# Optimization experiments

Hardware: AMD Instinct MI355X
Metric: run time of the kernel (lower is better)

## Reference

```python
import jax, jax.numpy as jnp
import numpy as np

N = 500_000
H = 256          # hidden_channels
A = 64           # aggr_channels
K = 5            # number of aggregators: sum, min, max, mean, std
B = 8192         # num graphs (segments)


def setup_inputs() -> dict:
    key = jax.random.key(0)
    k1, k2, k3, k4 = jax.random.split(key, 4)
    x = jax.random.normal(k1, (N, H), dtype=jnp.float32)
    batch = jnp.sort(jax.random.randint(k2, (N,), 0, B)).astype(jnp.int64)
    # Linear weights (stored input-major so forward is x @ W)
    W1 = jax.random.normal(k3, (H, A * K), dtype=jnp.float32) * (1.0 / np.sqrt(H))
    W2 = jax.random.normal(k4, (A * K, H), dtype=jnp.float32) * (1.0 / np.sqrt(A * K))
    b = jnp.zeros((H,), dtype=jnp.float32)
    return {"x": x, "batch": batch, "num_graphs": B, "W1": W1, "W2": W2, "b": b}


def reference(x, batch, num_graphs, W1, W2, b):
    # lin_aggr (no bias), then chunk into 5 pieces of width A along features
    h = x @ W1                                   # [N, 5A]
    h_sum, h_min, h_max, h_mean, h_std = jnp.split(h, K, axis=1)

    seg = batch.astype(jnp.int32)
    cnt = jax.ops.segment_sum(jnp.ones((x.shape[0], 1), x.dtype), seg,
                              num_segments=num_graphs)            # [B, 1]
    cnt = jnp.maximum(cnt, 1.0)

    z_sum = jax.ops.segment_sum(h_sum, seg, num_segments=num_graphs)
    z_min = jax.ops.segment_min(h_min, seg, num_segments=num_graphs)
    z_max = jax.ops.segment_max(h_max, seg, num_segments=num_graphs)
    z_mean = jax.ops.segment_sum(h_mean, seg, num_segments=num_graphs) / cnt
    # std via E[x^2] - E[x]^2 (PyG StdAggregation), clamped for stability
    m = jax.ops.segment_sum(h_std, seg, num_segments=num_graphs) / cnt
    m2 = jax.ops.segment_sum(h_std * h_std, seg, num_segments=num_graphs) / cnt
    z_std = jnp.sqrt(jnp.maximum(m2 - m * m, 1e-5))

    z = jnp.concatenate([z_sum, z_min, z_max, z_mean, z_std], axis=1)  # [B, 5A]
    return z @ W2 + b                                                   # [B, H]
```

## Files before the change

### kernel.cpp

```cpp
#include <hip/hip_runtime.h>
#include <hip/hip_bf16.h>
#include <float.h>
#include <stdint.h>

typedef __attribute__((ext_vector_type(8))) short bf16x8;
typedef __attribute__((ext_vector_type(4))) float f32x4;

#define NCH 320
#define NCG 20
#define GEMM_GRID 1024

static __device__ __forceinline__ unsigned short f2bf(float f) {
    union { float f; unsigned int u; } v; v.f = f;
    unsigned int u = v.u;
    u += 0x7FFFu + ((u >> 16) & 1u);
    return (unsigned short)(u >> 16);
}

static __device__ __forceinline__ float bf2f(unsigned short h) {
    union { unsigned int u; float f; } v; v.u = ((unsigned int)h) << 16;
    return v.f;
}

__global__ void seg_start_kernel(const int* __restrict__ batch,
                                 int* __restrict__ seg, int n, int b_gr) {
    int b = blockIdx.x * blockDim.x + threadIdx.x;
    if (b > b_gr) return;
    int lo = 0, hi = n;
    while (lo < hi) {
        int mid = (lo + hi) >> 1;
        if (batch[mid] < b) lo = mid + 1; else hi = mid;
    }
    seg[b] = lo;
}

__global__ void pack_w1_kernel(const float* __restrict__ W1,
                               unsigned short* __restrict__ w1p) {
    int idx = blockIdx.x * blockDim.x + threadIdx.x;
    if (idx >= NCG * 8 * 64) return;
    int lane = idx & 63;
    int ks = (idx >> 6) & 7;
    int cg = idx >> 9;
    int col = cg * 16 + (lane & 15);
    int kbase = ks * 32 + (lane >> 4) * 8;
    unsigned short* dst = w1p + (size_t)idx * 8;
#pragma unroll
    for (int j = 0; j < 8; ++j)
        dst[j] = f2bf(W1[(size_t)(kbase + j) * NCH + col]);
}

__global__ __launch_bounds__(512)
__attribute__((amdgpu_waves_per_eu(2, 2)))
void gemm_h_kernel(const float* __restrict__ x,
                   const unsigned short* __restrict__ w1p,
                   unsigned short* __restrict__ h,
                   int n, int nchunks, int span) {
    __shared__ unsigned short xs[64 * 256];

    const int tid = threadIdx.x;
    const int lane = tid & 63;
    const int w = tid >> 6;
    const int rg = lane >> 4;
    const int col = lane & 15;
    const int chA = w * 16 + col;
    const int chB = (w + 8) * 16 + col;
    const int chS = (16 + (w & 3)) * 16 + col;
    const int sthalf = w >> 2;

    const bf16x8* wp = (const bf16x8*)w1p;
    bf16x8 B0[8], B1[8], Bs[8];
#pragma unroll
    for (int ks = 0; ks < 8; ++ks) {
        B0[ks] = wp[(w * 8 + ks) * 64 + lane];
        B1[ks] = wp[((w + 8) * 8 + ks) * 64 + lane];
        Bs[ks] = wp[((16 + (w & 3)) * 8 + ks) * 64 + lane];
        asm volatile("" : "+v"(B0[ks]));
        asm volatile("" : "+v"(B1[ks]));
        asm volatile("" : "+v"(Bs[ks]));
    }

    int addrk[8];
#pragma unroll
    for (int ks = 0; ks < 8; ++ks)
        addrk[ks] = ((col * 512) + (rg * 16) + ks * 64) ^ ((col & 7) << 4);

    const float4* xv = (const float4*)x;
    const int c0 = blockIdx.x * span;
    const int c1 = min(c0 + span, nchunks);
    if (c0 >= c1) return;

#define LD8(CH) { const int base_ = (CH) << 6; \
        const int rem_ = min(n - base_, 64); \
        _Pragma("unroll") \
        for (int i_ = 0; i_ < 8; ++i_) { \
            int q_ = tid + i_ * 512; int row_ = q_ >> 6; \
            p[i_] = make_float4(0.f, 0.f, 0.f, 0.f); \
            if (row_ < rem_) p[i_] = xv[(size_t)(base_ + row_) * 64 + (q_ & 63)]; } }

#define ST8() { \
        _Pragma("unroll") \
        for (int i_ = 0; i_ < 8; ++i_) { \
            int q_ = tid + i_ * 512; int row_ = q_ >> 6; \
            int byt_ = ((row_ * 512) + ((q_ & 63) * 8)) ^ ((row_ & 7) << 4); \
            __hip_bfloat162 lo2_ = __float22bfloat162_rn(make_float2(p[i_].x, p[i_].y)); \
            __hip_bfloat162 hi2_ = __float22bfloat162_rn(make_float2(p[i_].z, p[i_].w)); \
            unsigned int ulo_, uhi_; \
            __builtin_memcpy(&ulo_, &lo2_, 4); __builtin_memcpy(&uhi_, &hi2_, 4); \
            *(uint2*)((char*)xs + byt_) = make_uint2(ulo_, uhi_); } }

    {
        float4 p[8];
        LD8(c0)
        ST8()
    }
    __syncthreads();

    for (int tc = c0; tc < c1; ++tc) {
        const bool more = (tc + 1 < c1);
        float4 p[8];
        if (more) LD8(tc + 1)
        const int base = tc << 6;
#pragma unroll
        for (int ps = 0; ps < 2; ++ps) {
            f32x4 aA0 = {0,0,0,0}, aA1 = {0,0,0,0};
            f32x4 aB0 = {0,0,0,0}, aB1 = {0,0,0,0};
            f32x4 aS0 = {0,0,0,0}, aS1 = {0,0,0,0};
            const char* pb = (const char*)xs + ps * 16384;
            const bool dostd = (sthalf == ps);
#pragma unroll
            for (int ks = 0; ks < 8; ++ks) {
                bf16x8 x0 = *(const bf16x8*)(pb + addrk[ks]);
                bf16x8 x1 = *(const bf16x8*)(pb + addrk[ks] + 8192);
                aA0 = __builtin_amdgcn_mfma_f32_16x16x32_bf16(x0, B0[ks], aA0, 0, 0, 0);
                aB0 = __builtin_amdgcn_mfma_f32_16x16x32_bf16(x0, B1[ks], aB0, 0, 0, 0);
                aA1 = __builtin_amdgcn_mfma_f32_16x16x32_bf16(x1, B0[ks], aA1, 0, 0, 0);
                aB1 = __builtin_amdgcn_mfma_f32_16x16x32_bf16(x1, B1[ks], aB1, 0, 0, 0);
                if (dostd) {
                    aS0 = __builtin_amdgcn_mfma_f32_16x16x32_bf16(x0, Bs[ks], aS0, 0, 0, 0);
                    aS1 = __builtin_amdgcn_mfma_f32_16x16x32_bf16(x1, Bs[ks], aS1, 0, 0, 0);
                }
            }
            const int rb0 = base + ps * 32 + rg * 4;
            const int rb1 = rb0 + 16;
            unsigned short* hp0 = h + (size_t)(rb0 >> 2) * 1280;
            unsigned short* hp1 = h + (size_t)(rb1 >> 2) * 1280;
#define STG(ACC, CH, HP) { \
            __hip_bfloat162 lo2 = __float22bfloat162_rn(make_float2((ACC)[0], (ACC)[1])); \
            __hip_bfloat162 hi2 = __float22bfloat162_rn(make_float2((ACC)[2], (ACC)[3])); \
            uint2 pk2; \
            __builtin_memcpy(&pk2.x, &lo2, 4); __builtin_memcpy(&pk2.y, &hi2, 4); \
            *(uint2*)((HP) + (CH) * 4) = pk2; }
            STG(aA0, chA, hp0)
            STG(aA1, chA, hp1)
            STG(aB0, chB, hp0)
            STG(aB1, chB, hp1)
            if (dostd) {
                STG(aS0, chS, hp0)
                STG(aS1, chS, hp1)
            }
#undef STG
        }
        __syncthreads();
        if (more) {
            ST8()
            __syncthreads();
        }
    }
#undef LD8
#undef ST8
}

__global__ __launch_bounds__(320) void reduce_kernel(
    const unsigned short* __restrict__ h, const int* __restrict__ seg,
    float* __restrict__ z) {
    const int g = blockIdx.x;
    const int sg = seg[g], en = seg[g + 1];
    const int cnt = en - sg;
    const int t = threadIdx.x;

    float s = 0.f, q = 0.f, mn = FLT_MAX, mx = -FLT_MAX;
    if (cnt > 0) {
        const unsigned short* hp = h + (size_t)t * 4;
        const int b40 = sg >> 2, b41 = (en - 1) >> 2;
        for (int b4 = b40; b4 <= b41; ++b4) {
            uint2 u = *(const uint2*)(hp + (size_t)b4 * 1280);
            const int r0 = b4 << 2;
#pragma unroll
            for (int j = 0; j < 4; ++j) {
                unsigned short e = (j < 2)
                    ? (unsigned short)((j == 0) ? (u.x & 0xFFFFu) : (u.x >> 16))
                    : (unsigned short)((j == 2) ? (u.y & 0xFFFFu) : (u.y >> 16));
                float v = bf2f(e);
                bool inr = (r0 + j >= sg) && (r0 + j < en);
                s += inr ? v : 0.f;
                q += inr ? v * v : 0.f;
                mn = fminf(mn, inr ? v : FLT_MAX);
                mx = fmaxf(mx, inr ? v : -FLT_MAX);
            }
        }
    }
    const float cntf = (float)max(cnt, 1);
    const int a = t >> 6;
    float res;
    if (a == 0) res = s;
    else if (a == 1) res = mn;
    else if (a == 2) res = mx;
    else if (a == 3) res = s / cntf;
    else {
        float m1 = s / cntf, m2 = q / cntf;
        res = sqrtf(fmaxf(m2 - m1 * m1, 1e-5f));
    }
    z[(size_t)g * NCH + t] = res;
}

__global__ __launch_bounds__(256) void k2_kernel(
    const float* __restrict__ z, const float* __restrict__ W2,
    const float* __restrict__ bias, float* __restrict__ out) {
    __shared__ float zf[NCH][17];
    const int g0 = blockIdx.x * 16;
    const int tid = threadIdx.x;
    for (int idx = tid; idx < 16 * NCH; idx += 256) {
        int m = idx / NCH;
        int c = idx - m * NCH;
        zf[c][m] = z[(size_t)(g0 + m) * NCH + c];
    }
    __syncthreads();
    float acc[16];
#pragma unroll
    for (int m = 0; m < 16; ++m) acc[m] = 0.f;
    for (int k = 0; k < NCH; ++k) {
        float wv = W2[(size_t)k * 256 + tid];
#pragma unroll
        for (int m = 0; m < 16; ++m) acc[m] += zf[k][m] * wv;
    }
    float bv = bias[tid];
#pragma unroll
    for (int m = 0; m < 16; ++m)
        out[(size_t)(g0 + m) * 256 + tid] = acc[m] + bv;
}

extern "C" void kernel_launch(void* const* d_in, const int* in_sizes, int n_in,
                              void* d_out, int out_size, void* d_ws, size_t ws_size,
                              hipStream_t stream) {
    const float* x = (const float*)d_in[0];
    const int* batch = (const int*)d_in[1];
    const float* W1 = (const float*)d_in[3];
    const float* W2 = (const float*)d_in[4];
    const float* bias = (const float*)d_in[5];

    const int n = in_sizes[1];
    const int b_gr = out_size / 256;
    const int nchunks = (n + 63) >> 6;
    const int span = (nchunks + GEMM_GRID - 1) / GEMM_GRID;

    char* ws = (char*)d_ws;
    unsigned short* w1p = (unsigned short*)ws;
    int* seg = (int*)(ws + 163840);
    float* z = (float*)(ws + 262144);
    unsigned short* h = (unsigned short*)(ws + 262144 +
                         (size_t)b_gr * NCH * sizeof(float));

    seg_start_kernel<<<(b_gr + 256) / 256, 256, 0, stream>>>(batch, seg, n, b_gr);
    pack_w1_kernel<<<(NCG * 8 * 64 + 255) / 256, 256, 0, stream>>>(W1, w1p);
    gemm_h_kernel<<<GEMM_GRID, 512, 0, stream>>>(x, w1p, h, n, nchunks, span);
    reduce_kernel<<<b_gr, 320, 0, stream>>>(h, seg, z);
    k2_kernel<<<b_gr / 16, 256, 0, stream>>>(z, W2, bias, (float*)d_out);
}
```

Before: 398.6 us.

## Double-buffer LDS tiles and prefetch two chunks ahead in GEMM kernel

Converts the GEMM's single LDS tile into two ping-pong buffers and keeps two register prefetch sets, so global loads for chunk tc+2 are in flight while chunk tc is computed. Barriers become raw s_barrier calls with lgkmcnt waits instead of __syncthreads. The grid is halved so each block runs more chunks and the deeper pipeline has more to overlap. In exchange it doubles LDS use and raises register pressure, which may limit occupancy.

```diff
diff --git a/kernel.cpp b/kernel.cpp
--- a/kernel.cpp
+++ b/kernel.cpp
@@ -8,7 +8,7 @@
 
 #define NCH 320
 #define NCG 20
-#define GEMM_GRID 1024
+#define GEMM_GRID 512
 
 static __device__ __forceinline__ unsigned short f2bf(float f) {
     union { float f; unsigned int u; } v; v.f = f;
@@ -55,7 +55,7 @@
                    const unsigned short* __restrict__ w1p,
                    unsigned short* __restrict__ h,
                    int n, int nchunks, int span) {
-    __shared__ unsigned short xs[64 * 256];
+    __shared__ unsigned short xs[2][64 * 256];
 
     const int tid = threadIdx.x;
     const int lane = tid & 63;
@@ -89,85 +89,99 @@
     const int c1 = min(c0 + span, nchunks);
     if (c0 >= c1) return;
 
-#define LD8(CH) { const int base_ = (CH) << 6; \
-        const int rem_ = min(n - base_, 64); \
+#define LGKBAR { asm volatile("s_waitcnt lgkmcnt(0)" ::: "memory"); \
+                 __builtin_amdgcn_s_barrier(); \
+                 asm volatile("" ::: "memory"); }
+
+#define LDM(P, CH) { const int ch_ = (CH); const int base_ = ch_ << 6; \
+        const int rem_ = (ch_ < c1) ? min(n - base_, 64) : 0; \
         _Pragma("unroll") \
         for (int i_ = 0; i_ < 8; ++i_) { \
             int q_ = tid + i_ * 512; int row_ = q_ >> 6; \
-            p[i_] = make_float4(0.f, 0.f, 0.f, 0.f); \
-            if (row_ < rem_) p[i_] = xv[(size_t)(base_ + row_) * 64 + (q_ & 63)]; } }
-
-#define ST8() { \
+            P[i_] = make_float4(0.f, 0.f, 0.f, 0.f); \
+            if (row_ < rem_) P[i_] = xv[(size_t)(base_ + row_) * 64 + (q_ & 63)]; } }
+
+#define STM(P, BUF) { \
         _Pragma("unroll") \
         for (int i_ = 0; i_ < 8; ++i_) { \
             int q_ = tid + i_ * 512; int row_ = q_ >> 6; \
             int byt_ = ((row_ * 512) + ((q_ & 63) * 8)) ^ ((row_ & 7) << 4); \
-            __hip_bfloat162 lo2_ = __float22bfloat162_rn(make_float2(p[i_].x, p[i_].y)); \
-            __hip_bfloat162 hi2_ = __float22bfloat162_rn(make_float2(p[i_].z, p[i_].w)); \
+            __hip_bfloat162 lo2_ = __float22bfloat162_rn(make_float2(P[i_].x, P[i_].y)); \
+            __hip_bfloat162 hi2_ = __float22bfloat162_rn(make_float2(P[i_].z, P[i_].w)); \
             unsigned int ulo_, uhi_; \
             __builtin_memcpy(&ulo_, &lo2_, 4); __builtin_memcpy(&uhi_, &hi2_, 4); \
-            *(uint2*)((char*)xs + byt_) = make_uint2(ulo_, uhi_); } }
-
-    {
-        float4 p[8];
-        LD8(c0)
-        ST8()
-    }
-    __syncthreads();
-
-    for (int tc = c0; tc < c1; ++tc) {
-        const bool more = (tc + 1 < c1);
-        float4 p[8];
-        if (more) LD8(tc + 1)
-        const int base = tc << 6;
-#pragma unroll
-        for (int ps = 0; ps < 2; ++ps) {
-            f32x4 aA0 = {0,0,0,0}, aA1 = {0,0,0,0};
-            f32x4 aB0 = {0,0,0,0}, aB1 = {0,0,0,0};
-            f32x4 aS0 = {0,0,0,0}, aS1 = {0,0,0,0};
-            const char* pb = (const char*)xs + ps * 16384;
-            const bool dostd = (sthalf == ps);
-#pragma unroll
-            for (int ks = 0; ks < 8; ++ks) {
-                bf16x8 x0 = *(const bf16x8*)(pb + addrk[ks]);
-                bf16x8 x1 = *(const bf16x8*)(pb + addrk[ks] + 8192);
-                aA0 = __builtin_amdgcn_mfma_f32_16x16x32_bf16(x0, B0[ks], aA0, 0, 0, 0);
-                aB0 = __builtin_amdgcn_mfma_f32_16x16x32_bf16(x0, B1[ks], aB0, 0, 0, 0);
-                aA1 = __builtin_amdgcn_mfma_f32_16x16x32_bf16(x1, B0[ks], aA1, 0, 0, 0);
-                aB1 = __builtin_amdgcn_mfma_f32_16x16x32_bf16(x1, B1[ks], aB1, 0, 0, 0);
-                if (dostd) {
-                    aS0 = __builtin_amdgcn_mfma_f32_16x16x32_bf16(x0, Bs[ks], aS0, 0, 0, 0);
-                    aS1 = __builtin_amdgcn_mfma_f32_16x16x32_bf16(x1, Bs[ks], aS1, 0, 0, 0);
-                }
-            }
-            const int rb0 = base + ps * 32 + rg * 4;
-            const int rb1 = rb0 + 16;
-            unsigned short* hp0 = h + (size_t)(rb0 >> 2) * 1280;
-            unsigned short* hp1 = h + (size_t)(rb1 >> 2) * 1280;
+            *(uint2*)((char*)(xs[BUF]) + byt_) = make_uint2(ulo_, uhi_); } }
+
+#define COMPUTE(TC, BUF) { \
+        const int base = (TC) << 6; \
+        _Pragma("unroll") \
+        for (int ps = 0; ps < 2; ++ps) { \
+            f32x4 aA0 = {0,0,0,0}, aA1 = {0,0,0,0}; \
+            f32x4 aB0 = {0,0,0,0}, aB1 = {0,0,0,0}; \
+            f32x4 aS0 = {0,0,0,0}, aS1 = {0,0,0,0}; \
+            const char* pb = (const char*)(xs[BUF]) + ps * 16384; \
+            const bool dostd = (sthalf == ps); \
+            _Pragma("unroll") \
+            for (int ks = 0; ks < 8; ++ks) { \
+                bf16x8 x0 = *(const bf16x8*)(pb + addrk[ks]); \
+                bf16x8 x1 = *(const bf16x8*)(pb + addrk[ks] + 8192); \
+                aA0 = __builtin_amdgcn_mfma_f32_16x16x32_bf16(x0, B0[ks], aA0, 0, 0, 0); \
+                aB0 = __builtin_amdgcn_mfma_f32_16x16x32_bf16(x0, B1[ks], aB0, 0, 0, 0); \
+                aA1 = __builtin_amdgcn_mfma_f32_16x16x32_bf16(x1, B0[ks], aA1, 0, 0, 0); \
+                aB1 = __builtin_amdgcn_mfma_f32_16x16x32_bf16(x1, B1[ks], aB1, 0, 0, 0); \
+                if (dostd) { \
+                    aS0 = __builtin_amdgcn_mfma_f32_16x16x32_bf16(x0, Bs[ks], aS0, 0, 0, 0); \
+                    aS1 = __builtin_amdgcn_mfma_f32_16x16x32_bf16(x1, Bs[ks], aS1, 0, 0, 0); \
+                } \
+            } \
+            const int rb0 = base + ps * 32 + rg * 4; \
+            const int rb1 = rb0 + 16; \
+            unsigned short* hp0 = h + (size_t)(rb0 >> 2) * 1280; \
+            unsigned short* hp1 = h + (size_t)(rb1 >> 2) * 1280; \
+            STG(aA0, chA, hp0) \
+            STG(aA1, chA, hp1) \
+            STG(aB0, chB, hp0) \
+            STG(aB1, chB, hp1) \
+            if (dostd) { \
+                STG(aS0, chS, hp0) \
+                STG(aS1, chS, hp1) \
+            } \
+        } }
+
 #define STG(ACC, CH, HP) { \
-            __hip_bfloat162 lo2 = __float22bfloat162_rn(make_float2((ACC)[0], (ACC)[1])); \
-            __hip_bfloat162 hi2 = __float22bfloat162_rn(make_float2((ACC)[2], (ACC)[3])); \
-            uint2 pk2; \
-            __builtin_memcpy(&pk2.x, &lo2, 4); __builtin_memcpy(&pk2.y, &hi2, 4); \
-            *(uint2*)((HP) + (CH) * 4) = pk2; }
-            STG(aA0, chA, hp0)
-            STG(aA1, chA, hp1)
-            STG(aB0, chB, hp0)
-            STG(aB1, chB, hp1)
-            if (dostd) {
-                STG(aS0, chS, hp0)
-                STG(aS1, chS, hp1)
-            }
+        __hip_bfloat162 lo2 = __float22bfloat162_rn(make_float2((ACC)[0], (ACC)[1])); \
+        __hip_bfloat162 hi2 = __float22bfloat162_rn(make_float2((ACC)[2], (ACC)[3])); \
+        uint2 pk2; \
+        __builtin_memcpy(&pk2.x, &lo2, 4); __builtin_memcpy(&pk2.y, &hi2, 4); \
+        *(uint2*)((HP) + (CH) * 4) = pk2; }
+
+    float4 pA[8], pB[8];
+    LDM(pA, c0)
+    LDM(pB, c0 + 1)
+    STM(pA, 0)
+    LGKBAR
+
+    int tc = c0;
+    while (true) {
+        if (tc + 2 < c1) LDM(pA, tc + 2)
+        COMPUTE(tc, 0)
+        LGKBAR
+        if (tc + 1 < c1) STM(pB, 1)
+        LGKBAR
+        ++tc; if (tc >= c1) break;
+
+        if (tc + 2 < c1) LDM(pB, tc + 2)
+        COMPUTE(tc, 1)
+        LGKBAR
+        if (tc + 1 < c1) STM(pA, 0)
+        LGKBAR
+        ++tc; if (tc >= c1) break;
+    }
+#undef LGKBAR
+#undef LDM
+#undef STM
+#undef COMPUTE
 #undef STG
-        }
-        __syncthreads();
-        if (more) {
-            ST8()
-            __syncthreads();
-        }
-    }
-#undef LD8
-#undef ST8
 }
 
 __global__ __launch_bounds__(320) void reduce_kernel(
```

After: 350.1 us. 1.14x faster.
